# Kernel optimization log

Hardware: AMD Instinct MI355X
Metric: run time of the kernel (lower is better)

Reference implementation:

```python
import jax, jax.numpy as jnp
import numpy as np

D_MODEL = 512
INF = 1e9
TEMP = np.sqrt(D_MODEL).astype(np.float32)


def setup_inputs() -> dict:
    key = jax.random.key(0)
    kq, kk, kv, km = jax.random.split(key, 4)
    B, L, D = 64, 1024, 64  # B = batch*heads
    q = jax.random.normal(kq, (B, L, D), dtype=jnp.float32)
    k = jax.random.normal(kk, (B, L, D), dtype=jnp.float32)
    v = jax.random.normal(kv, (B, L, D), dtype=jnp.float32)
    attn_mask = jax.random.randint(km, (B, L, L), 0, 2).astype(jnp.bool_)
    return {"q": q, "k": k, "v": v, "attn_mask": attn_mask}


def reference(q, k, v, attn_mask):
    # scores: [b, len_q, len_k]
    attn = jnp.einsum('bqd,bkd->bqk', q, k) / TEMP
    attn = jnp.where(attn_mask, -INF, attn)
    attn = jax.nn.softmax(attn, axis=2)
    # dropout p=0.0 -> identity
    out = jnp.einsum('bqk,bkd->bqd', attn, v)
    return out
```

## Files before the change

### kernel.cpp

```cpp
#include <hip/hip_runtime.h>
#include <hip/hip_bf16.h>


typedef __attribute__((ext_vector_type(4))) float f32x4;
typedef __attribute__((ext_vector_type(8))) short bf16x8;
typedef __attribute__((ext_vector_type(4))) short short4v;

constexpr int B_ = 64;
constexpr int L_ = 1024;
constexpr int D_ = 64;
constexpr int QBLK = 64;
constexpr int KV = 64;
constexpr int NKV = L_ / KV;
constexpr int PAD = 8;
constexpr int STR = KV + PAD;
constexpr int STRB = 72;
constexpr float INV_TEMP = 0.04419417382415922f;
constexpr float NEG = -1e9f;

__device__ inline short f2bf(float f) {
  __hip_bfloat16 h = __float2bfloat16(f);
  short s; __builtin_memcpy(&s, &h, 2);
  return s;
}

__global__ __launch_bounds__(256) void attn_fwd(
    const float* __restrict__ Q, const float* __restrict__ K,
    const float* __restrict__ V, const int* __restrict__ M,
    float* __restrict__ O)
{
  __shared__ short k_lds[KV][STR];
  __shared__ short vt_lds[D_][STR];
  __shared__ short p_lds[4][16][STR];
  __shared__ unsigned char m_lds[QBLK][STRB];

  const int qt   = blockIdx.x;
  const int b    = blockIdx.y;
  const int tid  = threadIdx.x;
  const int w    = tid >> 6;
  const int lane = tid & 63;
  const int g    = lane >> 4;
  const int c    = lane & 15;

  const int q0 = qt * QBLK;

  bf16x8 qf[2];
  {
    const int qrow = q0 + w * 16 + c;
    const float* qp = Q + ((size_t)b * L_ + qrow) * D_ + g * 8;
#pragma unroll
    for (int ks = 0; ks < 2; ++ks) {
      f32x4 x0 = *(const f32x4*)(qp + ks * 32);
      f32x4 x1 = *(const f32x4*)(qp + ks * 32 + 4);
      bf16x8 t;
      t[0] = f2bf(x0[0]); t[1] = f2bf(x0[1]); t[2] = f2bf(x0[2]); t[3] = f2bf(x0[3]);
      t[4] = f2bf(x1[0]); t[5] = f2bf(x1[1]); t[6] = f2bf(x1[2]); t[7] = f2bf(x1[3]);
      qf[ks] = t;
    }
  }

  const float* Kb = K + (size_t)b * L_ * D_;
  const float* Vb = V + (size_t)b * L_ * D_;
  const int*   Mb = M + (size_t)b * L_ * L_ + (size_t)q0 * L_;

  f32x4 acc[4];
#pragma unroll
  for (int i = 0; i < 4; ++i) acc[i] = (f32x4){0.f, 0.f, 0.f, 0.f};
  float m_run[4] = {-INFINITY, -INFINITY, -INFINITY, -INFINITY};
  float l_run[4] = {0.f, 0.f, 0.f, 0.f};

  for (int t = 0; t < NKV; ++t) {
    const int k0 = t * KV;

    {
      const float* ksrc = Kb + (size_t)k0 * D_;
      const float* vsrc = Vb + (size_t)k0 * D_;
      const int*   msrc = Mb + k0;
#pragma unroll
      for (int i = 0; i < 4; ++i) {
        const int idx = tid + i * 256;
        const int key = idx >> 4;
        const int d4  = (idx & 15) * 4;
        f32x4 kx = *(const f32x4*)(ksrc + (size_t)idx * 4);
        short4v ks4 = { f2bf(kx[0]), f2bf(kx[1]), f2bf(kx[2]), f2bf(kx[3]) };
        *(short4v*)&k_lds[key][d4] = ks4;
        f32x4 vx = *(const f32x4*)(vsrc + (size_t)idx * 4);
        vt_lds[d4 + 0][key] = f2bf(vx[0]);
        vt_lds[d4 + 1][key] = f2bf(vx[1]);
        vt_lds[d4 + 2][key] = f2bf(vx[2]);
        vt_lds[d4 + 3][key] = f2bf(vx[3]);
        const int4 mm = *(const int4*)(msrc + (size_t)key * L_ + d4);
        unsigned int packed = (unsigned int)(mm.x != 0)
                            | ((unsigned int)(mm.y != 0) << 8)
                            | ((unsigned int)(mm.z != 0) << 16)
                            | ((unsigned int)(mm.w != 0) << 24);
        *(unsigned int*)&m_lds[key][d4] = packed;
      }
    }
    __syncthreads();

    f32x4 sc[4];
#pragma unroll
    for (int f = 0; f < 4; ++f) {
      f32x4 a = (f32x4){0.f, 0.f, 0.f, 0.f};
#pragma unroll
      for (int ks = 0; ks < 2; ++ks) {
        bf16x8 kf = *(const bf16x8*)&k_lds[f * 16 + c][ks * 32 + g * 8];
        a = __builtin_amdgcn_mfma_f32_16x16x32_bf16(qf[ks], kf, a, 0, 0, 0);
      }
      sc[f] = a;
    }

#pragma unroll
    for (int f = 0; f < 4; ++f) {
#pragma unroll
      for (int r = 0; r < 4; ++r) {
        unsigned char mm = m_lds[w * 16 + g * 4 + r][f * 16 + c];
        sc[f][r] = mm ? NEG : sc[f][r] * INV_TEMP;
      }
    }

    float m_new[4], alpha[4];
#pragma unroll
    for (int r = 0; r < 4; ++r) {
      float x = fmaxf(fmaxf(sc[0][r], sc[1][r]), fmaxf(sc[2][r], sc[3][r]));
#pragma unroll
      for (int sh = 1; sh < 16; sh <<= 1) x = fmaxf(x, __shfl_xor(x, sh, 64));
      m_new[r] = fmaxf(m_run[r], x);
      alpha[r] = __expf(m_run[r] - m_new[r]);
    }
#pragma unroll
    for (int f = 0; f < 4; ++f)
#pragma unroll
      for (int r = 0; r < 4; ++r)
        sc[f][r] = __expf(sc[f][r] - m_new[r]);
#pragma unroll
    for (int r = 0; r < 4; ++r) {
      float s = (sc[0][r] + sc[1][r]) + (sc[2][r] + sc[3][r]);
#pragma unroll
      for (int sh = 1; sh < 16; sh <<= 1) s += __shfl_xor(s, sh, 64);
      l_run[r] = l_run[r] * alpha[r] + s;
      m_run[r] = m_new[r];
    }
#pragma unroll
    for (int fd = 0; fd < 4; ++fd)
#pragma unroll
      for (int r = 0; r < 4; ++r) acc[fd][r] *= alpha[r];

#pragma unroll
    for (int f = 0; f < 4; ++f)
#pragma unroll
      for (int r = 0; r < 4; ++r)
        p_lds[w][g * 4 + r][f * 16 + c] = f2bf(sc[f][r]);

#pragma unroll
    for (int ks = 0; ks < 2; ++ks) {
      bf16x8 pa = *(const bf16x8*)&p_lds[w][c][ks * 32 + g * 8];
#pragma unroll
      for (int fd = 0; fd < 4; ++fd) {
        bf16x8 vb = *(const bf16x8*)&vt_lds[fd * 16 + c][ks * 32 + g * 8];
        acc[fd] = __builtin_amdgcn_mfma_f32_16x16x32_bf16(pa, vb, acc[fd], 0, 0, 0);
      }
    }
    __syncthreads();
  }

  float inv_l[4];
#pragma unroll
  for (int r = 0; r < 4; ++r) inv_l[r] = 1.0f / l_run[r];
  float* orow = O + ((size_t)b * L_ + q0 + w * 16 + g * 4) * D_;
#pragma unroll
  for (int fd = 0; fd < 4; ++fd)
#pragma unroll
    for (int r = 0; r < 4; ++r)
      orow[(size_t)r * D_ + fd * 16 + c] = acc[fd][r] * inv_l[r];
}

extern "C" void kernel_launch(void* const* d_in, const int* in_sizes, int n_in,
                              void* d_out, int out_size, void* d_ws, size_t ws_size,
                              hipStream_t stream) {
  const float* q = (const float*)d_in[0];
  const float* k = (const float*)d_in[1];
  const float* v = (const float*)d_in[2];
  const int* m = (const int*)d_in[3];
  float* o = (float*)d_out;
  dim3 grid(L_ / QBLK, B_);
  attn_fwd<<<grid, 256, 0, stream>>>(q, k, v, m, o);
}
```

Baseline: 116.4 us.

## Prefetch next K/V/mask tile into registers while computing current tile

Splits the tile load into a global-to-register stage issued at the start of each iteration for the next tile and an LDS write stage after compute, so global memory latency overlaps the MFMA and softmax work. It also rotates the order of the transposed V stores per thread to reduce LDS bank conflicts. The cost is 48 extra registers per thread for staging, which may lower occupancy, plus an extra barrier per iteration.

```diff
diff --git a/kernel.cpp b/kernel.cpp
--- a/kernel.cpp
+++ b/kernel.cpp
@@ -63,41 +63,62 @@
   const float* Vb = V + (size_t)b * L_ * D_;
   const int*   Mb = M + (size_t)b * L_ * L_ + (size_t)q0 * L_;
 
+  f32x4 kreg[4], vreg[4];
+  int4  mreg[4];
+
+  auto stage_load = [&](int t) {
+    const float* ksrc = Kb + (size_t)(t * KV) * D_;
+    const float* vsrc = Vb + (size_t)(t * KV) * D_;
+    const int*   msrc = Mb + t * KV;
+#pragma unroll
+    for (int i = 0; i < 4; ++i) {
+      const int idx = tid + i * 256;
+      const int key = idx >> 4;
+      const int d4  = (idx & 15) * 4;
+      kreg[i] = *(const f32x4*)(ksrc + (size_t)idx * 4);
+      vreg[i] = *(const f32x4*)(vsrc + (size_t)idx * 4);
+      mreg[i] = *(const int4*)(msrc + (size_t)key * L_ + d4);
+    }
+  };
+
+  auto stage_write = [&]() {
+    const int rot = (tid & 15) >> 1;
+#pragma unroll
+    for (int i = 0; i < 4; ++i) {
+      const int idx = tid + i * 256;
+      const int key = idx >> 4;
+      const int d4  = (idx & 15) * 4;
+      f32x4 kx = kreg[i];
+      short4v ks4 = { f2bf(kx[0]), f2bf(kx[1]), f2bf(kx[2]), f2bf(kx[3]) };
+      *(short4v*)&k_lds[key][d4] = ks4;
+      f32x4 vx = vreg[i];
+#pragma unroll
+      for (int j = 0; j < 4; ++j) {
+        const int jj = (j + rot) & 3;
+        vt_lds[d4 + jj][key] = f2bf(vx[jj]);
+      }
+      int4 mm = mreg[i];
+      unsigned int packed = (unsigned int)(mm.x != 0)
+                          | ((unsigned int)(mm.y != 0) << 8)
+                          | ((unsigned int)(mm.z != 0) << 16)
+                          | ((unsigned int)(mm.w != 0) << 24);
+      *(unsigned int*)&m_lds[key][d4] = packed;
+    }
+  };
+
   f32x4 acc[4];
 #pragma unroll
   for (int i = 0; i < 4; ++i) acc[i] = (f32x4){0.f, 0.f, 0.f, 0.f};
   float m_run[4] = {-INFINITY, -INFINITY, -INFINITY, -INFINITY};
   float l_run[4] = {0.f, 0.f, 0.f, 0.f};
 
+  stage_load(0);
+  stage_write();
+  __syncthreads();
+
   for (int t = 0; t < NKV; ++t) {
-    const int k0 = t * KV;
-
-    {
-      const float* ksrc = Kb + (size_t)k0 * D_;
-      const float* vsrc = Vb + (size_t)k0 * D_;
-      const int*   msrc = Mb + k0;
-#pragma unroll
-      for (int i = 0; i < 4; ++i) {
-        const int idx = tid + i * 256;
-        const int key = idx >> 4;
-        const int d4  = (idx & 15) * 4;
-        f32x4 kx = *(const f32x4*)(ksrc + (size_t)idx * 4);
-        short4v ks4 = { f2bf(kx[0]), f2bf(kx[1]), f2bf(kx[2]), f2bf(kx[3]) };
-        *(short4v*)&k_lds[key][d4] = ks4;
-        f32x4 vx = *(const f32x4*)(vsrc + (size_t)idx * 4);
-        vt_lds[d4 + 0][key] = f2bf(vx[0]);
-        vt_lds[d4 + 1][key] = f2bf(vx[1]);
-        vt_lds[d4 + 2][key] = f2bf(vx[2]);
-        vt_lds[d4 + 3][key] = f2bf(vx[3]);
-        const int4 mm = *(const int4*)(msrc + (size_t)key * L_ + d4);
-        unsigned int packed = (unsigned int)(mm.x != 0)
-                            | ((unsigned int)(mm.y != 0) << 8)
-                            | ((unsigned int)(mm.z != 0) << 16)
-                            | ((unsigned int)(mm.w != 0) << 24);
-        *(unsigned int*)&m_lds[key][d4] = packed;
-      }
-    }
-    __syncthreads();
+    const bool has_next = (t + 1 < NKV);
+    if (has_next) stage_load(t + 1);
 
     f32x4 sc[4];
 #pragma unroll
@@ -162,6 +183,9 @@
         acc[fd] = __builtin_amdgcn_mfma_f32_16x16x32_bf16(pa, vb, acc[fd], 0, 0, 0);
       }
     }
+
+    __syncthreads();
+    if (has_next) stage_write();
     __syncthreads();
   }
 
```

Measured after the change: 104.8 us. 1.11x faster.
